# Optimization experiments

Measured on AMD Instinct MI355X. Metric: run time of the kernel, lower is better.

## Reference

```python
import jax, jax.numpy as jnp
import numpy as np

N_HEADS = 16
ROPE_THETA = 10000.0


def setup_inputs() -> dict:
    B, T, C = 4, 2048, 2048
    hd = C // N_HEADS  # 128
    key = jax.random.key(0)
    k1, k2, k3 = jax.random.split(key, 3)
    x = jax.random.normal(k1, (B, T, C), dtype=jnp.float32)
    # RoPE frequencies: angle[t, j] = t / theta^(2j/hd)
    inv_freq = 1.0 / (ROPE_THETA ** (jnp.arange(0, hd, 2, dtype=jnp.float32) / hd))  # (hd/2,)
    angles = jnp.arange(T, dtype=jnp.float32)[:, None] * inv_freq[None, :]  # (T, hd/2)
    freqs_cos = jnp.cos(angles)
    freqs_sin = jnp.sin(angles)
    W_qkv = jax.random.normal(k2, (C, 3 * C), dtype=jnp.float32) * (C ** -0.5)
    W_out = jax.random.normal(k3, (C, C), dtype=jnp.float32) * (C ** -0.5)
    return {"x": x, "freqs_cos": freqs_cos, "freqs_sin": freqs_sin, "W_qkv": W_qkv, "W_out": W_out}


def _apply_rope(t, cos, sin):
    # t: (B, H, T, hd); cos/sin: (T, hd/2). Interleaved-pair rotation, matching
    # torch view_as_complex on reshape(..., hd/2, 2).
    hd = t.shape[-1]
    tr = t.reshape(*t.shape[:-1], hd // 2, 2)
    x0, x1 = tr[..., 0], tr[..., 1]  # (B, H, T, hd/2)
    o0 = x0 * cos - x1 * sin
    o1 = x0 * sin + x1 * cos
    return jnp.stack([o0, o1], axis=-1).reshape(t.shape)


def reference(x, freqs_cos, freqs_sin, W_qkv, W_out):
    B, T, C = x.shape
    H = N_HEADS
    hd = C // H
    qkv = x @ W_qkv  # (B, T, 3C)
    q, k, v = jnp.split(qkv, 3, axis=-1)

    def heads(t):
        return t.reshape(B, T, H, hd).transpose(0, 2, 1, 3)  # (B, H, T, hd)

    cos, sin = freqs_cos[:T], freqs_sin[:T]
    q = _apply_rope(heads(q), cos, sin)
    k = _apply_rope(heads(k), cos, sin)
    v = heads(v)

    scale = hd ** -0.5
    scores = jnp.einsum('bhqd,bhkd->bhqk', q, k) * scale  # (B, H, T, T)
    causal = jnp.tril(jnp.ones((T, T), dtype=bool))
    scores = jnp.where(causal, scores, jnp.finfo(scores.dtype).min)
    attn = jax.nn.softmax(scores, axis=-1)
    out = jnp.einsum('bhqk,bhkd->bhqd', attn, v)  # (B, H, T, hd)
    out = out.transpose(0, 2, 1, 3).reshape(B, T, C)
    return out @ W_out, k, v
```

## Files before the change

### kernel.cpp

```cpp
#include <hip/hip_runtime.h>
#include <cstdint>
#include <cstddef>

typedef __attribute__((ext_vector_type(8))) short bf16x8;
typedef __attribute__((ext_vector_type(4))) float f32x4;

__device__ __forceinline__ unsigned short f2bf(float f) {
  union { float f; unsigned u; } v; v.f = f;
  unsigned r = v.u + 0x7FFFu + ((v.u >> 16) & 1u);
  return (unsigned short)(r >> 16);
}

#define GLL(gp, lp) __builtin_amdgcn_global_load_lds( \
    (const __attribute__((address_space(1))) void*)(gp), \
    (__attribute__((address_space(3))) void*)(lp), 16, 0, 0)

__global__ void cvt_x_kernel(const float* __restrict__ x, unsigned short* __restrict__ xb, int n4) {
  int i = blockIdx.x * blockDim.x + threadIdx.x;
  if (i >= n4) return;
  const float4 v = reinterpret_cast<const float4*>(x)[i];
  ushort4 o;
  o.x = f2bf(v.x); o.y = f2bf(v.y); o.z = f2bf(v.z); o.w = f2bf(v.w);
  reinterpret_cast<ushort4*>(xb)[i] = o;
}

__global__ void transpose_kernel(const float* __restrict__ src, unsigned short* __restrict__ dst,
                                 int K, int N) {
  __shared__ float t[32][33];
  const int tx = threadIdx.x, ty = threadIdx.y;
  const int n0 = blockIdx.x * 32, k0 = blockIdx.y * 32;
#pragma unroll
  for (int i = 0; i < 4; ++i)
    t[ty + i * 8][tx] = src[(size_t)(k0 + ty + i * 8) * N + n0 + tx];
  __syncthreads();
#pragma unroll
  for (int i = 0; i < 4; ++i)
    dst[(size_t)(n0 + ty + i * 8) * K + k0 + tx] = f2bf(t[tx][ty + i * 8]);
}

template <int EPI>
__global__ void gemm_bf16_kernel(
    const unsigned short* __restrict__ A, const unsigned short* __restrict__ B,
    int M, int N, int K,
    float* __restrict__ yout,
    const float* __restrict__ fcos, const float* __restrict__ fsin,
    unsigned short* __restrict__ q_ws, unsigned short* __restrict__ k_ws,
    unsigned short* __restrict__ vT_ws,
    float* __restrict__ k_out, float* __restrict__ v_out) {
  __shared__ unsigned short lsa[128 * 32];
  __shared__ unsigned short lsb[128 * 32];
  const int tid = threadIdx.x;
  const int w = tid >> 6, lane = tid & 63;
  const int wr = w >> 1, wc = w & 1;
  const int m0 = blockIdx.x * 128, n0 = blockIdx.y * 128;

  f32x4 acc[4][4] = {};

  const int stageRow = w * 32 + (lane >> 2);
  const int stageCol = (lane & 3) * 8;
  const unsigned short* aBase = A + (size_t)(m0 + stageRow) * K + stageCol;
  const unsigned short* bBase = B + (size_t)(n0 + stageRow) * K + stageCol;
  unsigned short* la = &lsa[(w * 32) * 32];
  unsigned short* lb = &lsb[(w * 32) * 32];

  const int kIters = K >> 5;
  for (int kk = 0; kk < kIters; ++kk) {
    const int k0 = kk << 5;
    __syncthreads();
    GLL(aBase + k0, la);
    GLL(aBase + (size_t)16 * K + k0, la + 16 * 32);
    GLL(bBase + k0, lb);
    GLL(bBase + (size_t)16 * K + k0, lb + 16 * 32);
    __syncthreads();
    bf16x8 af[4], bfr[4];
#pragma unroll
    for (int i = 0; i < 4; ++i)
      af[i] = *(const bf16x8*)&lsa[(wr * 64 + i * 16 + (lane & 15)) * 32 + (lane >> 4) * 8];
#pragma unroll
    for (int j = 0; j < 4; ++j)
      bfr[j] = *(const bf16x8*)&lsb[(wc * 64 + j * 16 + (lane & 15)) * 32 + (lane >> 4) * 8];
#pragma unroll
    for (int i = 0; i < 4; ++i)
#pragma unroll
      for (int j = 0; j < 4; ++j)
        acc[i][j] = __builtin_amdgcn_mfma_f32_16x16x32_bf16(af[i], bfr[j], acc[i][j], 0, 0, 0);
  }

  const int bn = blockIdx.y;
#pragma unroll
  for (int i = 0; i < 4; ++i) {
#pragma unroll
    for (int j = 0; j < 4; ++j) {
#pragma unroll
      for (int r = 0; r < 4; ++r) {
        const int m = m0 + wr * 64 + i * 16 + (lane >> 4) * 4 + r;
        const int n = n0 + wc * 64 + j * 16 + (lane & 15);
        const float val = acc[i][j][r];
        if (EPI == 0) {
          yout[(size_t)m * N + n] = val;
        } else {
          const int region = bn >> 4;
          const int h = bn & 15;
          const int b = m >> 11, t = m & 2047;
          const int dcol = n & 127;
          const size_t idx = ((size_t)((b * 16 + h) * 2048 + t)) * 128 + dcol;
          if (region == 2) {
            v_out[idx] = val;
            vT_ws[((size_t)(b * 16 + h) * 128 + dcol) * 2048 + t] = f2bf(val);
          } else {
            const int fi = dcol >> 1;
            const float c = fcos[t * 64 + fi];
            const float s = fsin[t * 64 + fi];
            const float part = __shfl_xor(val, 1);
            const float ro = (dcol & 1) ? (part * s + val * c) : (val * c - part * s);
            if (region == 0) {
              q_ws[idx] = f2bf(ro * 0.08838834764831845f);
            } else {
              k_out[idx] = ro;
              k_ws[idx] = f2bf(ro);
            }
          }
        }
      }
    }
  }
}

__global__ __launch_bounds__(256, 2) void attn_kernel(
    const unsigned short* __restrict__ q_ws,
    const unsigned short* __restrict__ k_ws,
    const unsigned short* __restrict__ vT_ws,
    unsigned short* __restrict__ attnout) {
  __shared__ unsigned short Kl[2][64 * 128];
  __shared__ unsigned short Vl[2][128 * 64];
  __shared__ unsigned short Pl[4][2][16 * 64];

  const int tid = threadIdx.x;
  const int w = tid >> 6, lane = tid & 63;
  const int g = lane >> 4, q16 = lane & 15;
  const int bh = blockIdx.x;
  const int qt = 15 - (int)blockIdx.y;
  const int b = bh >> 4, h = bh & 15;
  const int qbase = qt * 128;
  const int qb = qbase + w * 32;
  const size_t kvbase = (size_t)bh * 2048 * 128;

  const int krow_l = lane >> 4, kchunk = lane & 15;
  const int vrow_l = lane >> 3, vchunk = lane & 7;

  bf16x8 qf[2][4];
#pragma unroll
  for (int qs = 0; qs < 2; ++qs)
#pragma unroll
    for (int c = 0; c < 4; ++c)
      qf[qs][c] = *(const bf16x8*)&q_ws[kvbase + (size_t)(qb + qs * 16 + q16) * 128 + c * 32 + g * 8];

  f32x4 acc[2][8] = {};
  float mrun[2] = {-1e30f, -1e30f};
  float lrun[2] = {0.f, 0.f};

  const int nt = (qt + 1) * 2;

  auto stageK = [&](int buf, int kt) {
#pragma unroll
    for (int i = 0; i < 4; ++i) {
      const int slab = w * 4 + i;
      const int krow = slab * 4 + krow_l;
      GLL(k_ws + kvbase + (size_t)(kt + krow) * 128 + ((kchunk ^ (krow & 7)) << 3),
          ((unsigned short*)Kl[buf]) + slab * 512);
    }
  };
  auto stageV = [&](int buf, int kt) {
#pragma unroll
    for (int i = 0; i < 4; ++i) {
      const int slab = w * 4 + i;
      const int d = slab * 8 + vrow_l;
      GLL(vT_ws + kvbase + (size_t)d * 2048 + kt + ((vchunk ^ (d & 7)) << 3),
          ((unsigned short*)Vl[buf]) + slab * 512);
    }
  };

  stageK(0, 0); stageV(0, 0);
  int cur = 0;
  for (int it = 0; it < nt; ++it) {
    const int kt = it * 64;
    __syncthreads();
    if (it + 1 < nt) { stageK(cur ^ 1, kt + 64); stageV(cur ^ 1, kt + 64); }

    if (kt <= qb + 31) {
      f32x4 s[2][4];
#pragma unroll
      for (int qs = 0; qs < 2; ++qs)
#pragma unroll
        for (int t = 0; t < 4; ++t) s[qs][t] = f32x4{0.f, 0.f, 0.f, 0.f};
#pragma unroll
      for (int t = 0; t < 4; ++t) {
        const int key = t * 16 + q16;
#pragma unroll
        for (int c = 0; c < 4; ++c) {
          bf16x8 kf = *(const bf16x8*)&Kl[cur][key * 128 + (((c * 4 + g) ^ (key & 7)) << 3)];
          s[0][t] = __builtin_amdgcn_mfma_f32_16x16x32_bf16(kf, qf[0][c], s[0][t], 0, 0, 0);
          s[1][t] = __builtin_amdgcn_mfma_f32_16x16x32_bf16(kf, qf[1][c], s[1][t], 0, 0, 0);
        }
      }

#pragma unroll
      for (int qs = 0; qs < 2; ++qs) {
        const int qrow = qb + qs * 16 + q16;
        if (kt + 64 > qb + qs * 16) {
#pragma unroll
          for (int t = 0; t < 4; ++t)
#pragma unroll
            for (int r = 0; r < 4; ++r)
              if (kt + t * 16 + g * 4 + r > qrow) s[qs][t][r] = -1e30f;
        }
        float tm = s[qs][0][0];
#pragma unroll
        for (int t = 0; t < 4; ++t)
#pragma unroll
          for (int r = 0; r < 4; ++r) tm = fmaxf(tm, s[qs][t][r]);
        tm = fmaxf(tm, __shfl_xor(tm, 16));
        tm = fmaxf(tm, __shfl_xor(tm, 32));
        if (__any(tm > mrun[qs] + 8.0f)) {
          const float mnew = fmaxf(mrun[qs], tm);
          const float fac = __expf(mrun[qs] - mnew);
          lrun[qs] *= fac;
          mrun[qs] = mnew;
          float fr0 = __shfl(fac, g * 4 + 0), fr1 = __shfl(fac, g * 4 + 1);
          float fr2 = __shfl(fac, g * 4 + 2), fr3 = __shfl(fac, g * 4 + 3);
#pragma unroll
          for (int n = 0; n < 8; ++n) {
            acc[qs][n][0] *= fr0; acc[qs][n][1] *= fr1;
            acc[qs][n][2] *= fr2; acc[qs][n][3] *= fr3;
          }
        }
        float ps = 0.f;
        unsigned pk[8];
#pragma unroll
        for (int t = 0; t < 4; ++t) {
          const float p0 = __expf(s[qs][t][0] - mrun[qs]);
          const float p1 = __expf(s[qs][t][1] - mrun[qs]);
          const float p2 = __expf(s[qs][t][2] - mrun[qs]);
          const float p3 = __expf(s[qs][t][3] - mrun[qs]);
          ps += (p0 + p1) + (p2 + p3);
          pk[t * 2]     = (unsigned)f2bf(p0) | ((unsigned)f2bf(p1) << 16);
          pk[t * 2 + 1] = (unsigned)f2bf(p2) | ((unsigned)f2bf(p3) << 16);
        }
        ps += __shfl_xor(ps, 16);
        ps += __shfl_xor(ps, 32);
        lrun[qs] += ps;
#pragma unroll
        for (int t = 0; t < 4; ++t) {
          const unsigned byteoff = (unsigned)(q16 * 128) +
              (((unsigned)(t * 32 + g * 8)) ^ ((unsigned)(q16 & 7) << 4));
          *(uint2*)((char*)&Pl[w][qs][0] + byteoff) = make_uint2(pk[t * 2], pk[t * 2 + 1]);
        }
      }

#pragma unroll
      for (int ks = 0; ks < 2; ++ks) {
        const unsigned pcol = ((unsigned)(ks * 64 + g * 16)) ^ ((unsigned)(q16 & 7) << 4);
        bf16x8 pa0 = *(const bf16x8*)((char*)&Pl[w][0][0] + q16 * 128 + pcol);
        bf16x8 pa1 = *(const bf16x8*)((char*)&Pl[w][1][0] + q16 * 128 + pcol);
#pragma unroll
        for (int n = 0; n < 8; ++n) {
          const int d = n * 16 + q16;
          bf16x8 vf = *(const bf16x8*)&Vl[cur][d * 64 + (((ks * 4 + g) ^ (d & 7)) << 3)];
          acc[0][n] = __builtin_amdgcn_mfma_f32_16x16x32_bf16(pa0, vf, acc[0][n], 0, 0, 0);
          acc[1][n] = __builtin_amdgcn_mfma_f32_16x16x32_bf16(pa1, vf, acc[1][n], 0, 0, 0);
        }
      }
    }
    cur ^= 1;
  }

#pragma unroll
  for (int qs = 0; qs < 2; ++qs) {
    float rl[4];
#pragma unroll
    for (int r = 0; r < 4; ++r) rl[r] = 1.0f / __shfl(lrun[qs], g * 4 + r);
#pragma unroll
    for (int n = 0; n < 8; ++n) {
#pragma unroll
      for (int r = 0; r < 4; ++r) {
        const int q = qb + qs * 16 + g * 4 + r;
        const int d = n * 16 + q16;
        attnout[((size_t)(b * 2048 + q)) * 2048 + h * 128 + d] = f2bf(acc[qs][n][r] * rl[r]);
      }
    }
  }
}

extern "C" void kernel_launch(void* const* d_in, const int* in_sizes, int n_in,
                              void* d_out, int out_size, void* d_ws, size_t ws_size,
                              hipStream_t stream) {
  (void)in_sizes; (void)n_in; (void)out_size; (void)ws_size;
  const float* x    = (const float*)d_in[0];
  const float* fcos = (const float*)d_in[1];
  const float* fsin = (const float*)d_in[2];
  const float* Wqkv = (const float*)d_in[3];
  const float* Wout = (const float*)d_in[4];

  float* out   = (float*)d_out;
  float* y_out = out;
  float* k_out = out + (size_t)16777216;
  float* v_out = out + (size_t)33554432;

  unsigned short* xb      = (unsigned short*)d_ws;
  unsigned short* wqkvT   = xb + 16777216;
  unsigned short* woutT   = wqkvT + 12582912;
  unsigned short* q_ws    = woutT + 4194304;
  unsigned short* k_ws    = q_ws + 16777216;
  unsigned short* vT_ws   = k_ws + 16777216;
  unsigned short* attnout = xb;

  cvt_x_kernel<<<16384, 256, 0, stream>>>(x, xb, 4194304);
  transpose_kernel<<<dim3(192, 64), dim3(32, 8), 0, stream>>>(Wqkv, wqkvT, 2048, 6144);
  transpose_kernel<<<dim3(64, 64), dim3(32, 8), 0, stream>>>(Wout, woutT, 2048, 2048);

  gemm_bf16_kernel<1><<<dim3(64, 48), 256, 0, stream>>>(
      xb, wqkvT, 8192, 6144, 2048,
      nullptr, fcos, fsin, q_ws, k_ws, vT_ws, k_out, v_out);

  attn_kernel<<<dim3(64, 16), 256, 0, stream>>>(q_ws, k_ws, vT_ws, attnout);

  gemm_bf16_kernel<0><<<dim3(64, 16), 256, 0, stream>>>(
      attnout, woutT, 8192, 2048, 2048,
      y_out, nullptr, nullptr, nullptr, nullptr, nullptr, nullptr, nullptr);
}
```

Baseline: 533.6 us.

## Replace GEMM with 256x256 tile, 8-wave, double-buffered pipelined kernel

```diff
diff --git a/kernel.cpp b/kernel.cpp
--- a/kernel.cpp
+++ b/kernel.cpp
@@ -14,6 +14,15 @@
 #define GLL(gp, lp) __builtin_amdgcn_global_load_lds( \
     (const __attribute__((address_space(1))) void*)(gp), \
     (__attribute__((address_space(3))) void*)(lp), 16, 0, 0)
+
+#define FENCE() __builtin_amdgcn_sched_barrier(0)
+
+#define BARRIER() do { \
+  asm volatile("" ::: "memory"); \
+  __builtin_amdgcn_sched_barrier(0); \
+  __builtin_amdgcn_s_barrier(); \
+  __builtin_amdgcn_sched_barrier(0); \
+  asm volatile("" ::: "memory"); } while (0)
 
 __global__ void cvt_x_kernel(const float* __restrict__ x, unsigned short* __restrict__ xb, int n4) {
   int i = blockIdx.x * blockDim.x + threadIdx.x;
@@ -38,79 +47,141 @@
     dst[(size_t)(n0 + ty + i * 8) * K + k0 + tx] = f2bf(t[tx][ty + i * 8]);
 }
 
+
+#define READA(DST, MQ) do { \
+  _Pragma("unroll") for (int i_ = 0; i_ < 4; ++i_) { \
+    const int row_ = wm * 128 + (MQ) * 64 + i_ * 16 + q16; \
+    _Pragma("unroll") for (int kh_ = 0; kh_ < 2; ++kh_) \
+      DST[i_][kh_] = *(const bf16x8*)(Ab + row_ * 128 + ((((kh_ << 2) | g) ^ (row_ & 7)) << 4)); \
+  } } while (0)
+
+#define READB(DST, NQ) do { \
+  _Pragma("unroll") for (int j_ = 0; j_ < 2; ++j_) { \
+    const int row_ = wn * 64 + (NQ) * 32 + j_ * 16 + q16; \
+    _Pragma("unroll") for (int kh_ = 0; kh_ < 2; ++kh_) \
+      DST[j_][kh_] = *(const bf16x8*)(Bb + row_ * 128 + ((((kh_ << 2) | g) ^ (row_ & 7)) << 4)); \
+  } } while (0)
+
+#define MFMAPH(AR, BR, MB, NB) do { \
+  __builtin_amdgcn_s_setprio(1); \
+  _Pragma("unroll") for (int i_ = 0; i_ < 4; ++i_) \
+  _Pragma("unroll") for (int j_ = 0; j_ < 2; ++j_) \
+  _Pragma("unroll") for (int kh_ = 0; kh_ < 2; ++kh_) \
+    acc[(MB) + i_][(NB) + j_] = __builtin_amdgcn_mfma_f32_16x16x32_bf16( \
+        AR[i_][kh_], BR[j_][kh_], acc[(MB) + i_][(NB) + j_], 0, 0, 0); \
+  __builtin_amdgcn_s_setprio(0); \
+  } while (0)
+
 template <int EPI>
-__global__ void gemm_bf16_kernel(
-    const unsigned short* __restrict__ A, const unsigned short* __restrict__ B,
-    int M, int N, int K,
+__global__ __launch_bounds__(512, 2) void gemm8_kernel(
+    const unsigned short* __restrict__ Ag, const unsigned short* __restrict__ Bg,
+    int K, int N, int mtMask, int mtShift,
     float* __restrict__ yout,
     const float* __restrict__ fcos, const float* __restrict__ fsin,
     unsigned short* __restrict__ q_ws, unsigned short* __restrict__ k_ws,
     unsigned short* __restrict__ vT_ws,
     float* __restrict__ k_out, float* __restrict__ v_out) {
-  __shared__ unsigned short lsa[128 * 32];
-  __shared__ unsigned short lsb[128 * 32];
+  __shared__ unsigned short Asb[2][16384];
+  __shared__ unsigned short Bsb[2][16384];
+
   const int tid = threadIdx.x;
   const int w = tid >> 6, lane = tid & 63;
-  const int wr = w >> 1, wc = w & 1;
-  const int m0 = blockIdx.x * 128, n0 = blockIdx.y * 128;
-
-  f32x4 acc[4][4] = {};
-
-  const int stageRow = w * 32 + (lane >> 2);
-  const int stageCol = (lane & 3) * 8;
-  const unsigned short* aBase = A + (size_t)(m0 + stageRow) * K + stageCol;
-  const unsigned short* bBase = B + (size_t)(n0 + stageRow) * K + stageCol;
-  unsigned short* la = &lsa[(w * 32) * 32];
-  unsigned short* lb = &lsb[(w * 32) * 32];
-
-  const int kIters = K >> 5;
-  for (int kk = 0; kk < kIters; ++kk) {
-    const int k0 = kk << 5;
-    __syncthreads();
-    GLL(aBase + k0, la);
-    GLL(aBase + (size_t)16 * K + k0, la + 16 * 32);
-    GLL(bBase + k0, lb);
-    GLL(bBase + (size_t)16 * K + k0, lb + 16 * 32);
-    __syncthreads();
-    bf16x8 af[4], bfr[4];
-#pragma unroll
-    for (int i = 0; i < 4; ++i)
-      af[i] = *(const bf16x8*)&lsa[(wr * 64 + i * 16 + (lane & 15)) * 32 + (lane >> 4) * 8];
-#pragma unroll
-    for (int j = 0; j < 4; ++j)
-      bfr[j] = *(const bf16x8*)&lsb[(wc * 64 + j * 16 + (lane & 15)) * 32 + (lane >> 4) * 8];
-#pragma unroll
-    for (int i = 0; i < 4; ++i)
-#pragma unroll
-      for (int j = 0; j < 4; ++j)
-        acc[i][j] = __builtin_amdgcn_mfma_f32_16x16x32_bf16(af[i], bfr[j], acc[i][j], 0, 0, 0);
+  const int wm = w >> 2, wn = w & 3;
+  const int g = lane >> 4, q16 = lane & 15;
+  const int ls = lane >> 3;
+  const int lc = ((lane & 7) ^ ls) << 3;
+
+  const int cpx = (int)gridDim.x >> 3;
+  int bid = (int)blockIdx.x;
+  bid = (bid & 7) * cpx + (bid >> 3);
+  const int bm = bid & mtMask;
+  const int bn = bid >> mtShift;
+  const int m0 = bm << 8, n0 = bn << 8;
+  const int NT = K >> 6;
+
+  auto stageA = [&](int tile, int half) {
+    if (tile >= NT) return;
+    const int rowbase = (w >> 2) * 128 + half * 64 + (w & 3) * 16;
+    unsigned short* base = &Asb[tile & 1][rowbase * 64];
+    const unsigned short* src = Ag + (size_t)(m0 + rowbase + ls) * K + tile * 64 + lc;
+#pragma unroll
+    for (int i = 0; i < 2; ++i)
+      GLL(src + (size_t)i * 8 * K, base + i * 8 * 64);
+  };
+  auto stageB = [&](int tile, int half) {
+    if (tile >= NT) return;
+#pragma unroll
+    for (int i = 0; i < 2; ++i) {
+      const int seq = w * 2 + i;
+      const int rowbase = (seq >> 2) * 64 + half * 32 + (seq & 3) * 8;
+      GLL(Bg + (size_t)(n0 + rowbase + ls) * K + tile * 64 + lc,
+          &Bsb[tile & 1][rowbase * 64]);
+    }
+  };
+
+  f32x4 acc[8][4] = {};
+  bf16x8 a[4][2], b0[2][2], b1[2][2];
+
+  stageA(0, 0); FENCE();
+  stageB(0, 0); FENCE();
+  stageB(0, 1); FENCE();
+  stageA(0, 1); FENCE();
+  stageA(1, 0); FENCE();
+  stageB(1, 0); FENCE();
+  stageB(1, 1); FENCE();
+  asm volatile("s_waitcnt vmcnt(6)" ::: "memory");
+  BARRIER();
+
+  for (int t = 0; t < NT; ++t) {
+    const char* Ab = (const char*)Asb + (t & 1) * 32768;
+    const char* Bb = (const char*)Bsb + (t & 1) * 32768;
+    READA(a, 0); READB(b0, 0);
+    stageA(t + 1, 1);
+    BARRIER();
+    MFMAPH(a, b0, 0, 0);
+    BARRIER();
+    READB(b1, 1);
+    stageA(t + 2, 0);
+    BARRIER();
+    MFMAPH(a, b1, 0, 2);
+    BARRIER();
+    READA(a, 1);
+    stageB(t + 2, 0);
+    BARRIER();
+    MFMAPH(a, b1, 4, 2);
+    BARRIER();
+    stageB(t + 2, 1);
+    if (t < NT - 2) { asm volatile("s_waitcnt vmcnt(6)" ::: "memory"); }
+    else           { asm volatile("s_waitcnt vmcnt(0)" ::: "memory"); }
+    BARRIER();
+    MFMAPH(a, b0, 4, 0);
+    BARRIER();
   }
 
-  const int bn = blockIdx.y;
-#pragma unroll
-  for (int i = 0; i < 4; ++i) {
-#pragma unroll
-    for (int j = 0; j < 4; ++j) {
+  const int region = n0 >> 11;
+#pragma unroll
+  for (int mi = 0; mi < 8; ++mi) {
+#pragma unroll
+    for (int nj = 0; nj < 4; ++nj) {
 #pragma unroll
       for (int r = 0; r < 4; ++r) {
-        const int m = m0 + wr * 64 + i * 16 + (lane >> 4) * 4 + r;
-        const int n = n0 + wc * 64 + j * 16 + (lane & 15);
-        const float val = acc[i][j][r];
+        const int m = m0 + wm * 128 + mi * 16 + g * 4 + r;
+        const int n = n0 + wn * 64 + nj * 16 + q16;
+        const float val = acc[mi][nj][r];
         if (EPI == 0) {
           yout[(size_t)m * N + n] = val;
         } else {
-          const int region = bn >> 4;
-          const int h = bn & 15;
-          const int b = m >> 11, t = m & 2047;
+          const int h = (n >> 7) & 15;
+          const int b = m >> 11, tt = m & 2047;
           const int dcol = n & 127;
-          const size_t idx = ((size_t)((b * 16 + h) * 2048 + t)) * 128 + dcol;
+          const size_t idx = ((size_t)((b * 16 + h) * 2048 + tt)) * 128 + dcol;
           if (region == 2) {
             v_out[idx] = val;
-            vT_ws[((size_t)(b * 16 + h) * 128 + dcol) * 2048 + t] = f2bf(val);
+            vT_ws[((size_t)(b * 16 + h) * 128 + dcol) * 2048 + tt] = f2bf(val);
           } else {
             const int fi = dcol >> 1;
-            const float c = fcos[t * 64 + fi];
-            const float s = fsin[t * 64 + fi];
+            const float c = fcos[tt * 64 + fi];
+            const float s = fsin[tt * 64 + fi];
             const float part = __shfl_xor(val, 1);
             const float ro = (dcol & 1) ? (part * s + val * c) : (val * c - part * s);
             if (region == 0) {
@@ -257,6 +328,8 @@
         }
       }
 
+      asm volatile("s_waitcnt lgkmcnt(0)" ::: "memory");
+      __builtin_amdgcn_sched_barrier(0);
 #pragma unroll
       for (int ks = 0; ks < 2; ++ks) {
         const unsigned pcol = ((unsigned)(ks * 64 + g * 16)) ^ ((unsigned)(q16 & 7) << 4);
@@ -318,13 +391,13 @@
   transpose_kernel<<<dim3(192, 64), dim3(32, 8), 0, stream>>>(Wqkv, wqkvT, 2048, 6144);
   transpose_kernel<<<dim3(64, 64), dim3(32, 8), 0, stream>>>(Wout, woutT, 2048, 2048);
 
-  gemm_bf16_kernel<1><<<dim3(64, 48), 256, 0, stream>>>(
-      xb, wqkvT, 8192, 6144, 2048,
+  gemm8_kernel<1><<<768, 512, 0, stream>>>(
+      xb, wqkvT, 2048, 6144, 31, 5,
       nullptr, fcos, fsin, q_ws, k_ws, vT_ws, k_out, v_out);
 
   attn_kernel<<<dim3(64, 16), 256, 0, stream>>>(q_ws, k_ws, vT_ws, attnout);
 
-  gemm_bf16_kernel<0><<<dim3(64, 16), 256, 0, stream>>>(
-      attnout, woutT, 8192, 2048, 2048,
+  gemm8_kernel<0><<<256, 512, 0, stream>>>(
+      attnout, woutT, 2048, 2048, 31, 5,
       y_out, nullptr, nullptr, nullptr, nullptr, nullptr, nullptr, nullptr);
 }
```

Measured after the change: 560.2 us. +5.0%, slower.

## Double-buffer GEMM LDS tiles with swizzle and XCD-aware block remap

Applied to the files above, without the earlier changes.

```diff
diff --git a/kernel.cpp b/kernel.cpp
--- a/kernel.cpp
+++ b/kernel.cpp
@@ -14,6 +14,19 @@
 #define GLL(gp, lp) __builtin_amdgcn_global_load_lds( \
     (const __attribute__((address_space(1))) void*)(gp), \
     (__attribute__((address_space(3))) void*)(lp), 16, 0, 0)
+
+#define BARRIER() do { \
+  __builtin_amdgcn_sched_barrier(0); \
+  __builtin_amdgcn_s_barrier(); \
+  __builtin_amdgcn_sched_barrier(0); } while (0)
+
+#define WAIT_LGKM0() do { \
+  asm volatile("s_waitcnt lgkmcnt(0)"); \
+  __builtin_amdgcn_sched_barrier(0); } while (0)
+
+#define WAIT_VM0() do { \
+  asm volatile("s_waitcnt vmcnt(0)"); \
+  __builtin_amdgcn_sched_barrier(0); } while (0)
 
 __global__ void cvt_x_kernel(const float* __restrict__ x, unsigned short* __restrict__ xb, int n4) {
   int i = blockIdx.x * blockDim.x + threadIdx.x;
@@ -38,79 +51,112 @@
     dst[(size_t)(n0 + ty + i * 8) * K + k0 + tx] = f2bf(t[tx][ty + i * 8]);
 }
 
+
 template <int EPI>
-__global__ void gemm_bf16_kernel(
-    const unsigned short* __restrict__ A, const unsigned short* __restrict__ B,
-    int M, int N, int K,
+__global__ void gemm2p_kernel(
+    const unsigned short* __restrict__ Ag, const unsigned short* __restrict__ Bg,
+    int K, int N, int mtMask, int mtShift,
     float* __restrict__ yout,
     const float* __restrict__ fcos, const float* __restrict__ fsin,
     unsigned short* __restrict__ q_ws, unsigned short* __restrict__ k_ws,
     unsigned short* __restrict__ vT_ws,
     float* __restrict__ k_out, float* __restrict__ v_out) {
-  __shared__ unsigned short lsa[128 * 32];
-  __shared__ unsigned short lsb[128 * 32];
+  __shared__ unsigned short Asb[2][128 * 32];
+  __shared__ unsigned short Bsb[2][128 * 32];
+
   const int tid = threadIdx.x;
   const int w = tid >> 6, lane = tid & 63;
   const int wr = w >> 1, wc = w & 1;
-  const int m0 = blockIdx.x * 128, n0 = blockIdx.y * 128;
+  const int g = lane >> 4, q16 = lane & 15;
+
+  const int cpx = (int)gridDim.x >> 3;
+  int bid = (int)blockIdx.x;
+  bid = (bid & 7) * cpx + (bid >> 3);
+  const int bm = bid & mtMask, bn = bid >> mtShift;
+  const int m0 = bm << 7, n0 = bn << 7;
+  const int NT = K >> 5;
+
+  const int srow = lane >> 2;
+  const int sslot = lane & 3;
+
+  auto stageA = [&](int tile) {
+    if (tile >= NT) return;
+    unsigned short* dst = &Asb[tile & 1][0];
+#pragma unroll
+    for (int j = 0; j < 2; ++j) {
+      const int row = w * 32 + j * 16 + srow;
+      const int c = sslot ^ ((row >> 1) & 3);
+      GLL(Ag + (size_t)(m0 + row) * K + tile * 32 + c * 8,
+          dst + (w * 32 + j * 16) * 32);
+    }
+  };
+  auto stageB = [&](int tile) {
+    if (tile >= NT) return;
+    unsigned short* dst = &Bsb[tile & 1][0];
+#pragma unroll
+    for (int j = 0; j < 2; ++j) {
+      const int row = w * 32 + j * 16 + srow;
+      const int c = sslot ^ ((row >> 1) & 3);
+      GLL(Bg + (size_t)(n0 + row) * K + tile * 32 + c * 8,
+          dst + (w * 32 + j * 16) * 32);
+    }
+  };
 
   f32x4 acc[4][4] = {};
 
-  const int stageRow = w * 32 + (lane >> 2);
-  const int stageCol = (lane & 3) * 8;
-  const unsigned short* aBase = A + (size_t)(m0 + stageRow) * K + stageCol;
-  const unsigned short* bBase = B + (size_t)(n0 + stageRow) * K + stageCol;
-  unsigned short* la = &lsa[(w * 32) * 32];
-  unsigned short* lb = &lsb[(w * 32) * 32];
-
-  const int kIters = K >> 5;
-  for (int kk = 0; kk < kIters; ++kk) {
-    const int k0 = kk << 5;
-    __syncthreads();
-    GLL(aBase + k0, la);
-    GLL(aBase + (size_t)16 * K + k0, la + 16 * 32);
-    GLL(bBase + k0, lb);
-    GLL(bBase + (size_t)16 * K + k0, lb + 16 * 32);
-    __syncthreads();
+  stageA(0); stageB(0);
+  WAIT_VM0();
+  BARRIER();
+
+  for (int t = 0; t < NT; ++t) {
+    stageA(t + 1); stageB(t + 1);
+    const unsigned short* Ab = Asb[t & 1];
+    const unsigned short* Bb = Bsb[t & 1];
     bf16x8 af[4], bfr[4];
 #pragma unroll
-    for (int i = 0; i < 4; ++i)
-      af[i] = *(const bf16x8*)&lsa[(wr * 64 + i * 16 + (lane & 15)) * 32 + (lane >> 4) * 8];
-#pragma unroll
-    for (int j = 0; j < 4; ++j)
-      bfr[j] = *(const bf16x8*)&lsb[(wc * 64 + j * 16 + (lane & 15)) * 32 + (lane >> 4) * 8];
+    for (int i = 0; i < 4; ++i) {
+      const int row = wr * 64 + i * 16 + q16;
+      af[i] = *(const bf16x8*)(Ab + row * 32 + ((g ^ ((row >> 1) & 3)) << 3));
+    }
+#pragma unroll
+    for (int j = 0; j < 4; ++j) {
+      const int row = wc * 64 + j * 16 + q16;
+      bfr[j] = *(const bf16x8*)(Bb + row * 32 + ((g ^ ((row >> 1) & 3)) << 3));
+    }
+    WAIT_LGKM0();
 #pragma unroll
     for (int i = 0; i < 4; ++i)
 #pragma unroll
       for (int j = 0; j < 4; ++j)
         acc[i][j] = __builtin_amdgcn_mfma_f32_16x16x32_bf16(af[i], bfr[j], acc[i][j], 0, 0, 0);
+    WAIT_VM0();
+    BARRIER();
   }
 
-  const int bn = blockIdx.y;
 #pragma unroll
   for (int i = 0; i < 4; ++i) {
 #pragma unroll
     for (int j = 0; j < 4; ++j) {
 #pragma unroll
       for (int r = 0; r < 4; ++r) {
-        const int m = m0 + wr * 64 + i * 16 + (lane >> 4) * 4 + r;
-        const int n = n0 + wc * 64 + j * 16 + (lane & 15);
+        const int m = m0 + wr * 64 + i * 16 + g * 4 + r;
+        const int n = n0 + wc * 64 + j * 16 + q16;
         const float val = acc[i][j][r];
         if (EPI == 0) {
           yout[(size_t)m * N + n] = val;
         } else {
           const int region = bn >> 4;
           const int h = bn & 15;
-          const int b = m >> 11, t = m & 2047;
+          const int b = m >> 11, tt = m & 2047;
           const int dcol = n & 127;
-          const size_t idx = ((size_t)((b * 16 + h) * 2048 + t)) * 128 + dcol;
+          const size_t idx = ((size_t)((b * 16 + h) * 2048 + tt)) * 128 + dcol;
           if (region == 2) {
             v_out[idx] = val;
-            vT_ws[((size_t)(b * 16 + h) * 128 + dcol) * 2048 + t] = f2bf(val);
+            vT_ws[((size_t)(b * 16 + h) * 128 + dcol) * 2048 + tt] = f2bf(val);
           } else {
             const int fi = dcol >> 1;
-            const float c = fcos[t * 64 + fi];
-            const float s = fsin[t * 64 + fi];
+            const float c = fcos[tt * 64 + fi];
+            const float s = fsin[tt * 64 + fi];
             const float part = __shfl_xor(val, 1);
             const float ro = (dcol & 1) ? (part * s + val * c) : (val * c - part * s);
             if (region == 0) {
@@ -257,6 +303,8 @@
         }
       }
 
+      asm volatile("s_waitcnt lgkmcnt(0)" ::: "memory");
+      __builtin_amdgcn_sched_barrier(0);
 #pragma unroll
       for (int ks = 0; ks < 2; ++ks) {
         const unsigned pcol = ((unsigned)(ks * 64 + g * 16)) ^ ((unsigned)(q16 & 7) << 4);
@@ -318,13 +366,13 @@
   transpose_kernel<<<dim3(192, 64), dim3(32, 8), 0, stream>>>(Wqkv, wqkvT, 2048, 6144);
   transpose_kernel<<<dim3(64, 64), dim3(32, 8), 0, stream>>>(Wout, woutT, 2048, 2048);
 
-  gemm_bf16_kernel<1><<<dim3(64, 48), 256, 0, stream>>>(
-      xb, wqkvT, 8192, 6144, 2048,
+  gemm2p_kernel<1><<<3072, 256, 0, stream>>>(
+      xb, wqkvT, 2048, 6144, 63, 6,
       nullptr, fcos, fsin, q_ws, k_ws, vT_ws, k_out, v_out);
 
   attn_kernel<<<dim3(64, 16), 256, 0, stream>>>(q_ws, k_ws, vT_ws, attnout);
 
-  gemm_bf16_kernel<0><<<dim3(64, 16), 256, 0, stream>>>(
-      attnout, woutT, 8192, 2048, 2048,
+  gemm2p_kernel<0><<<1024, 256, 0, stream>>>(
+      attnout, woutT, 2048, 2048, 63, 6,
       y_out, nullptr, nullptr, nullptr, nullptr, nullptr, nullptr, nullptr);
 }
```

Result: slower. 594.6 us (+11.4%).
